# Kernel optimization log

Hardware: AMD Instinct MI355X
Metric: run time of the kernel (lower is better)

Reference implementation:

```python
import jax, jax.numpy as jnp
import numpy as np

B, N, D = 1, 2048, 1024
H = 16
HD = D // H
MAX_REL = 100          # relative_positional_distance
NUM_EMB = 2 * MAX_REL - 1
NEG = 1e8


def _rel_pos_logits(q_pos, rel_emb):
    """Fairseq-style learned relative positional logits (unmasked).

    q_pos:   [L, B*H, hd]  (unscaled queries)
    rel_emb: [H, 2*MAX_REL-1, hd]
    returns: [B*H, L, L]
    """
    L = q_pos.shape[0]
    pad_len = max(L - MAX_REL, 0)
    start = max(MAX_REL - L, 0)
    # get_embeddings_for_query: pad to cover relative offsets -(L-1)..(L-1)
    padded = jnp.pad(rel_emb, ((0, 0), (pad_len, pad_len), (0, 0)))
    used = padded[:, start:start + 2 * L - 1, :]          # [H, 2L-1, hd]
    # calculate_positional_logits
    q4 = q_pos.reshape(L, -1, H, HD)                       # [L, B, H, hd]
    logits = jnp.einsum('lbhd,hmd->lbhm', q4, used)        # [L, B, H, 2L-1]
    logits = logits.reshape(L, -1, 2 * L - 1)              # [L, BH, 2L-1]
    if pad_len > 0:  # mask relative positions beyond max_relative_pos
        logits = logits.at[:, :, :pad_len].add(-NEG)
        logits = logits.at[:, :, -pad_len:].add(-NEG)
    # relative_to_absolute_indexing (unmasked skewing trick)
    bh = logits.shape[1]
    x = jnp.pad(logits, ((0, 0), (0, 0), (0, 1)))          # [L, BH, 2L]
    x = jnp.transpose(x, (1, 0, 2)).reshape(bh, L * 2 * L)
    x = jnp.pad(x, ((0, 0), (0, L - 1)))
    x = x.reshape(bh, L + 1, 2 * L - 1)
    return x[:, :L, L - 1:]                                # [BH, L, L]


def setup_inputs() -> dict:
    key = jax.random.key(0)
    ks = jax.random.split(key, 6)
    x = jax.random.normal(ks[0], (B, N, D), dtype=jnp.float32)
    qkv_w = jax.random.normal(ks[1], (3 * D, D), dtype=jnp.float32) * 0.02
    qkv_b = jnp.zeros((3 * D,), dtype=jnp.float32)
    proj_w = jax.random.normal(ks[2], (D, D), dtype=jnp.float32) * 0.02
    proj_b = jnp.zeros((D,), dtype=jnp.float32)
    rel_emb = jax.random.normal(ks[3], (H, NUM_EMB, HD), dtype=jnp.float32) * (HD ** -0.5)
    return {"x": x, "qkv_w": qkv_w, "qkv_b": qkv_b,
            "proj_w": proj_w, "proj_b": proj_b, "rel_emb": rel_emb}


def reference(x, qkv_w, qkv_b, proj_w, proj_b, rel_emb):
    b, n, d = x.shape
    qkv = x @ qkv_w.T + qkv_b                                # [B,N,3D]
    qkv = qkv.reshape(b, n, 3, H, HD).transpose(2, 0, 3, 1, 4)
    q, k, v = qkv[0], qkv[1], qkv[2]                          # [B,H,N,hd]
    scale = 1.0 / np.sqrt(HD).astype(np.float32)
    logits = jnp.einsum('bhqd,bhkd->bhqk', q, k) * scale      # [B,H,N,N]
    q_pos = jnp.transpose(q, (0, 2, 1, 3)).reshape(n, b * H, HD)
    pos = _rel_pos_logits(q_pos, rel_emb).reshape(b, H, n, n)
    probs = jax.nn.softmax(logits + pos, axis=-1)             # dropout off (eval)
    out = jnp.einsum('bhqk,bhkd->bhqd', probs, v)
    out = jnp.transpose(out, (0, 2, 1, 3)).reshape(b, n, d)
    return out @ proj_w.T + proj_b
```

## Files before the change

### kernel.cpp

```cpp
#include <hip/hip_runtime.h>
#include <hip/hip_bf16.h>

#define N_SEQ 2048
#define DMODEL 1024
#define NHEAD 16
#define HD 64
#define NREL 199

typedef __bf16 bf16x8 __attribute__((ext_vector_type(8)));
typedef float f32x4 __attribute__((ext_vector_type(4)));

__device__ __forceinline__ bf16x8 cvt8(float4 a, float4 b) {
    bf16x8 r;
    r[0] = (__bf16)a.x; r[1] = (__bf16)a.y; r[2] = (__bf16)a.z; r[3] = (__bf16)a.w;
    r[4] = (__bf16)b.x; r[5] = (__bf16)b.y; r[6] = (__bf16)b.z; r[7] = (__bf16)b.w;
    return r;
}

#define MFMA16(A, B, C) __builtin_amdgcn_mfma_f32_16x16x32_bf16(A, B, C, 0, 0, 0)

__device__ __forceinline__ void async_copy16(void* lds, const void* g) {
    __builtin_amdgcn_global_load_lds(
        (__attribute__((address_space(1))) unsigned int*)g,
        (__attribute__((address_space(3))) unsigned int*)lds, 16, 0, 0);
}

__global__ __launch_bounds__(256) void cvt3(
    const float* __restrict__ a, __bf16* __restrict__ ao, int na,
    const float* __restrict__ b, __bf16* __restrict__ bo, int nb,
    const float* __restrict__ c, __bf16* __restrict__ co)
{
    int i = (blockIdx.x * blockDim.x + threadIdx.x) * 8;
    const float* src; __bf16* dst;
    if (i < na)              { src = a + i;            dst = ao + i; }
    else if (i - na < nb)    { src = b + (i - na);     dst = bo + (i - na); }
    else                     { src = c + (i - na - nb); dst = co + (i - na - nb); }
    float4 f0 = ((const float4*)src)[0];
    float4 f1 = ((const float4*)src)[1];
    *(bf16x8*)dst = cvt8(f0, f1);
}

template<int BM, int BN, bool OUT_BF16>
__global__ __launch_bounds__(256) void gemm_bt64(
    const __bf16* __restrict__ A,
    const __bf16* __restrict__ W,
    const float* __restrict__ bias,
    void* __restrict__ Cout,
    int lda, int Nc, int K, int ldc)
{
    constexpr int RT = BM + BN;
    constexpr int WM = BM / 2, WN = BN / 2;
    constexpr int MI = WM / 16, NI = WN / 16;
    constexpr int CHUNKS = RT / 4 / 8;

    __shared__ __bf16 s[RT][64];

    const int tid  = threadIdx.x;
    const int wid  = tid >> 6;
    const int lane = tid & 63;
    const int quad = lane >> 4;
    const int l15  = lane & 15;
    const int wm   = (wid >> 1) * WM;
    const int wn   = (wid & 1) * WN;
    const int bm   = blockIdx.y * BM;
    const int bn   = blockIdx.x * BN;

    const int lrow = lane >> 3;
    const int lcb  = ((lane & 7) ^ lrow) * 8;

    f32x4 acc[MI][NI] = {};

    for (int k0 = 0; k0 < K; k0 += 64) {
        #pragma unroll
        for (int c = 0; c < CHUNKS; c++) {
            const int r0 = wid * (RT / 4) + c * 8;
            const __bf16* src = (r0 < BM)
                ? A + (size_t)(bm + r0 + lrow) * lda + k0 + lcb
                : W + (size_t)(bn + (r0 - BM) + lrow) * K + k0 + lcb;
            async_copy16(&s[r0][0], src);
        }
        __syncthreads();

        #pragma unroll
        for (int half = 0; half < 2; half++) {
            bf16x8 af[MI], bfr[NI];
            #pragma unroll
            for (int mi = 0; mi < MI; mi++) {
                int ar = wm + mi * 16 + l15;
                af[mi] = *(const bf16x8*)&s[ar][((quad + 4 * half) ^ (ar & 7)) * 8];
            }
            #pragma unroll
            for (int ni = 0; ni < NI; ni++) {
                int br = BM + wn + ni * 16 + l15;
                bfr[ni] = *(const bf16x8*)&s[br][((quad + 4 * half) ^ (br & 7)) * 8];
            }
            #pragma unroll
            for (int mi = 0; mi < MI; mi++)
                #pragma unroll
                for (int ni = 0; ni < NI; ni++)
                    acc[mi][ni] = MFMA16(af[mi], bfr[ni], acc[mi][ni]);
        }
        __syncthreads();
    }

    #pragma unroll
    for (int ni = 0; ni < NI; ni++) {
        int col = bn + wn + ni * 16 + l15;
        float bv = bias[col];
        #pragma unroll
        for (int mi = 0; mi < MI; mi++)
            #pragma unroll
            for (int ri = 0; ri < 4; ri++) {
                int row = bm + wm + mi * 16 + quad * 4 + ri;
                float v = acc[mi][ni][ri] + bv;
                if (OUT_BF16)
                    reinterpret_cast<__bf16*>(Cout)[(size_t)row * ldc + col] = (__bf16)v;
                else
                    reinterpret_cast<float*>(Cout)[(size_t)row * ldc + col] = v;
            }
    }
}

__global__ __launch_bounds__(256) void attn_band_mfma(
    __hip_bfloat16* __restrict__ qkv,
    const float* __restrict__ rel_emb)
{
    __shared__ __align__(16) char smem[53248];
    __bf16 (*q_s)[72]   = (__bf16(*)[72])smem;
    __bf16 (*p_s)[72]   = (__bf16(*)[72])smem;
    __bf16 (*P_s)[200]  = (__bf16(*)[200])(smem + 9216);
    __bf16 (*relc)[72]  = (__bf16(*)[72])(smem + 34816);
    __bf16 (*k_s)[72]   = (__bf16(*)[72])(smem + 34816);
    __bf16 (*v_s)[72]   = (__bf16(*)[72])(smem + 34816 + 9216);

    const int tid  = threadIdx.x;
    const int wid  = tid >> 6;
    const int lane = tid & 63;
    const int quad = lane >> 4;
    const int l15  = lane & 15;
    const int h    = blockIdx.x >> 5;
    const int q0   = (blockIdx.x & 31) * 64;
    const int srow = tid >> 2;
    const int sq   = (tid & 3) * 16;

    const int j_lo   = (q0 - 99 > 0) ? (q0 - 99) : 0;
    const int j_hi   = (q0 + 162 < N_SEQ - 1) ? (q0 + 162) : (N_SEQ - 1);
    const int ntiles = (j_hi - j_lo + 64) >> 6;

    {
        const __hip_bfloat16* src = qkv + (size_t)(q0 + srow) * 3072 + h * HD + sq;
        uint4 u0 = ((const uint4*)src)[0];
        uint4 u1 = ((const uint4*)src)[1];
        *(uint4*)&q_s[srow][sq]     = u0;
        *(uint4*)&q_s[srow][sq + 8] = u1;
    }
    for (int idx = tid; idx < 112 * 4; idx += 256) {
        int er = idx >> 2, ec = (idx & 3) * 16;
        const float4* s = (const float4*)(rel_emb + ((size_t)h * NREL + er) * HD + ec);
        float4 f0 = s[0], f1 = s[1], f2 = s[2], f3 = s[3];
        *(bf16x8*)&relc[er][ec]     = cvt8(f0, f1);
        *(bf16x8*)&relc[er][ec + 8] = cvt8(f2, f3);
    }
    __syncthreads();

    const bf16x8 aq0 = *(const bf16x8*)&q_s[wid * 16 + l15][quad * 8];
    const bf16x8 aq1 = *(const bf16x8*)&q_s[wid * 16 + l15][quad * 8 + 32];

    #pragma unroll
    for (int t = 0; t < 7; t++) {
        f32x4 pacc = {};
        bf16x8 b0 = *(const bf16x8*)&relc[t * 16 + l15][quad * 8];
        bf16x8 b1 = *(const bf16x8*)&relc[t * 16 + l15][quad * 8 + 32];
        pacc = MFMA16(aq0, b0, pacc);
        pacc = MFMA16(aq1, b1, pacc);
        #pragma unroll
        for (int ri = 0; ri < 4; ri++)
            P_s[wid * 16 + quad * 4 + ri][t * 16 + l15] = (__bf16)pacc[ri];
    }
    __syncthreads();

    for (int idx = tid; idx < 96 * 4; idx += 256) {
        int er = 112 + (idx >> 2); if (er > NREL - 1) er = NREL - 1;
        int ec = (idx & 3) * 16;
        const float4* s = (const float4*)(rel_emb + ((size_t)h * NREL + er) * HD + ec);
        float4 f0 = s[0], f1 = s[1], f2 = s[2], f3 = s[3];
        *(bf16x8*)&relc[idx >> 2][ec]     = cvt8(f0, f1);
        *(bf16x8*)&relc[idx >> 2][ec + 8] = cvt8(f2, f3);
    }
    __syncthreads();

    #pragma unroll
    for (int t = 7; t < 13; t++) {
        f32x4 pacc = {};
        bf16x8 b0 = *(const bf16x8*)&relc[t * 16 + l15 - 112][quad * 8];
        bf16x8 b1 = *(const bf16x8*)&relc[t * 16 + l15 - 112][quad * 8 + 32];
        pacc = MFMA16(aq0, b0, pacc);
        pacc = MFMA16(aq1, b1, pacc);
        #pragma unroll
        for (int ri = 0; ri < 4; ri++) {
            int col = t * 16 + l15;
            if (col < NREL)
                P_s[wid * 16 + quad * 4 + ri][col] = (__bf16)pacc[ri];
        }
    }

    bf16x8 bones;
    {
        __bf16 o = (l15 == 0) ? (__bf16)1.0f : (__bf16)0.0f;
        #pragma unroll
        for (int i = 0; i < 8; i++) bones[i] = o;
    }

    f32x4 O[4] = {};
    f32x4 Osum = {};

    for (int t = 0; t < ntiles; t++) {
        __syncthreads();
        const int j0 = j_lo + t * 64;
        {
            int jr = j0 + srow; if (jr > N_SEQ - 1) jr = N_SEQ - 1;
            const __hip_bfloat16* ks = qkv + (size_t)jr * 3072 + 1024 + h * HD + sq;
            uint4 k0 = ((const uint4*)ks)[0], k1 = ((const uint4*)ks)[1];
            *(uint4*)&k_s[srow][sq]     = k0;
            *(uint4*)&k_s[srow][sq + 8] = k1;
            const __hip_bfloat16* vsp = qkv + (size_t)jr * 3072 + 2048 + h * HD + sq;
            uint4 v0 = ((const uint4*)vsp)[0], v1 = ((const uint4*)vsp)[1];
            __bf16 vtmp[16];
            *(uint4*)&vtmp[0] = v0; *(uint4*)&vtmp[8] = v1;
            #pragma unroll
            for (int i = 0; i < 16; i++) v_s[sq + i][srow] = vtmp[i];
        }
        __syncthreads();

        f32x4 S[4] = {};
        #pragma unroll
        for (int nt = 0; nt < 4; nt++) {
            bf16x8 b0 = *(const bf16x8*)&k_s[nt * 16 + l15][quad * 8];
            bf16x8 b1 = *(const bf16x8*)&k_s[nt * 16 + l15][quad * 8 + 32];
            S[nt] = MFMA16(aq0, b0, S[nt]);
            S[nt] = MFMA16(aq1, b1, S[nt]);
        }

        #pragma unroll
        for (int nt = 0; nt < 4; nt++) {
            int jg = j0 + nt * 16 + l15;
            #pragma unroll
            for (int ri = 0; ri < 4; ri++) {
                int r_loc = wid * 16 + quad * 4 + ri;
                int e = jg - (q0 + r_loc) + 99;
                float v = -3.0e38f;
                if ((unsigned)e < (unsigned)NREL && jg < N_SEQ)
                    v = S[nt][ri] * 0.125f + (float)P_s[r_loc][e];
                float p = __expf(v);
                p_s[r_loc][nt * 16 + l15] = (__bf16)p;
            }
        }

        bf16x8 ap0 = *(const bf16x8*)&p_s[wid * 16 + l15][quad * 8];
        bf16x8 ap1 = *(const bf16x8*)&p_s[wid * 16 + l15][quad * 8 + 32];
        #pragma unroll
        for (int nt = 0; nt < 4; nt++) {
            bf16x8 b0 = *(const bf16x8*)&v_s[nt * 16 + l15][quad * 8];
            bf16x8 b1 = *(const bf16x8*)&v_s[nt * 16 + l15][quad * 8 + 32];
            O[nt] = MFMA16(ap0, b0, O[nt]);
            O[nt] = MFMA16(ap1, b1, O[nt]);
        }
        Osum = MFMA16(ap0, bones, Osum);
        Osum = MFMA16(ap1, bones, Osum);
    }

    #pragma unroll
    for (int ri = 0; ri < 4; ri++) {
        float s = __shfl(Osum[ri], (lane & 48), 64);
        float inv = 1.0f / s;
        #pragma unroll
        for (int nt = 0; nt < 4; nt++) {
            int r = q0 + wid * 16 + quad * 4 + ri;
            qkv[(size_t)r * 3072 + h * HD + nt * 16 + l15] =
                __float2bfloat16(O[nt][ri] * inv);
        }
    }
}

extern "C" void kernel_launch(void* const* d_in, const int* in_sizes, int n_in,
                              void* d_out, int out_size, void* d_ws, size_t ws_size,
                              hipStream_t stream)
{
    (void)out_size; (void)ws_size; (void)n_in;

    const float *x = nullptr, *qkv_w = nullptr, *qkv_b = nullptr;
    const float *proj_w = nullptr, *proj_b = nullptr, *rel = nullptr;
    for (int i = 0; i < 6; i++) {
        switch (in_sizes[i]) {
            case 2097152: x      = (const float*)d_in[i]; break;
            case 3145728: qkv_w  = (const float*)d_in[i]; break;
            case 3072:    qkv_b  = (const float*)d_in[i]; break;
            case 1048576: proj_w = (const float*)d_in[i]; break;
            case 1024:    proj_b = (const float*)d_in[i]; break;
            case 203776:  rel    = (const float*)d_in[i]; break;
            default: break;
        }
    }

    char* ws = (char*)d_ws;
    __hip_bfloat16* qkv = (__hip_bfloat16*)ws;
    __bf16* xb  = (__bf16*)(ws + 12582912);
    __bf16* wb  = (__bf16*)(ws + 16777216);
    __bf16* pwb = (__bf16*)(ws + 23068672);
    float* out = (float*)d_out;

    cvt3<<<dim3(6291456 / 8 / 256), 256, 0, stream>>>(
        x, xb, 2097152, qkv_w, wb, 3145728, proj_w, pwb);
    gemm_bt64<128, 64, true><<<dim3(3072 / 64, N_SEQ / 128), 256, 0, stream>>>(
        xb, wb, qkv_b, (void*)qkv, DMODEL, 3072, DMODEL, 3072);
    attn_band_mfma<<<dim3(NHEAD * (N_SEQ / 64)), 256, 0, stream>>>(qkv, rel);
    gemm_bt64<64, 64, false><<<dim3(DMODEL / 64, N_SEQ / 64), 256, 0, stream>>>(
        (const __bf16*)qkv, pwb, proj_b, (void*)out, 3072, DMODEL, DMODEL, DMODEL);
}
```

Baseline: 132.0 us.

## Double K-step in GEMMs and register-prefetch next K/V tile in attention

The GEMM kernel now loads two 64-wide K slices into shared memory per iteration, which halves the number of barrier pairs and lets more async loads be in flight at once. The band attention kernel now holds the next K/V tile in registers, loading it from global memory while the current tile is being computed. Both aim to hide global memory latency. The cost is double the GEMM shared memory, which may lower occupancy, plus extra registers in the attention kernel.

```diff
diff --git a/kernel.cpp b/kernel.cpp
--- a/kernel.cpp
+++ b/kernel.cpp
@@ -40,7 +40,7 @@
     *(bf16x8*)dst = cvt8(f0, f1);
 }
 
-template<int BM, int BN, bool OUT_BF16>
+template<int BM, int BN, int KS, bool OUT_BF16>
 __global__ __launch_bounds__(256) void gemm_bt64(
     const __bf16* __restrict__ A,
     const __bf16* __restrict__ W,
@@ -53,7 +53,7 @@
     constexpr int MI = WM / 16, NI = WN / 16;
     constexpr int CHUNKS = RT / 4 / 8;
 
-    __shared__ __bf16 s[RT][64];
+    __shared__ __bf16 s[KS][RT][64];
 
     const int tid  = threadIdx.x;
     const int wid  = tid >> 6;
@@ -70,36 +70,40 @@
 
     f32x4 acc[MI][NI] = {};
 
-    for (int k0 = 0; k0 < K; k0 += 64) {
-        #pragma unroll
-        for (int c = 0; c < CHUNKS; c++) {
-            const int r0 = wid * (RT / 4) + c * 8;
-            const __bf16* src = (r0 < BM)
-                ? A + (size_t)(bm + r0 + lrow) * lda + k0 + lcb
-                : W + (size_t)(bn + (r0 - BM) + lrow) * K + k0 + lcb;
-            async_copy16(&s[r0][0], src);
-        }
+    for (int k0 = 0; k0 < K; k0 += 64 * KS) {
+        #pragma unroll
+        for (int ks = 0; ks < KS; ks++)
+            #pragma unroll
+            for (int c = 0; c < CHUNKS; c++) {
+                const int r0 = wid * (RT / 4) + c * 8;
+                const __bf16* src = (r0 < BM)
+                    ? A + (size_t)(bm + r0 + lrow) * lda + k0 + ks * 64 + lcb
+                    : W + (size_t)(bn + (r0 - BM) + lrow) * K + k0 + ks * 64 + lcb;
+                async_copy16(&s[ks][r0][0], src);
+            }
         __syncthreads();
 
         #pragma unroll
-        for (int half = 0; half < 2; half++) {
-            bf16x8 af[MI], bfr[NI];
-            #pragma unroll
-            for (int mi = 0; mi < MI; mi++) {
-                int ar = wm + mi * 16 + l15;
-                af[mi] = *(const bf16x8*)&s[ar][((quad + 4 * half) ^ (ar & 7)) * 8];
+        for (int ks = 0; ks < KS; ks++)
+            #pragma unroll
+            for (int half = 0; half < 2; half++) {
+                bf16x8 af[MI], bfr[NI];
+                #pragma unroll
+                for (int mi = 0; mi < MI; mi++) {
+                    int ar = wm + mi * 16 + l15;
+                    af[mi] = *(const bf16x8*)&s[ks][ar][((quad + 4 * half) ^ (ar & 7)) * 8];
+                }
+                #pragma unroll
+                for (int ni = 0; ni < NI; ni++) {
+                    int br = BM + wn + ni * 16 + l15;
+                    bfr[ni] = *(const bf16x8*)&s[ks][br][((quad + 4 * half) ^ (br & 7)) * 8];
+                }
+                #pragma unroll
+                for (int mi = 0; mi < MI; mi++)
+                    #pragma unroll
+                    for (int ni = 0; ni < NI; ni++)
+                        acc[mi][ni] = MFMA16(af[mi], bfr[ni], acc[mi][ni]);
             }
-            #pragma unroll
-            for (int ni = 0; ni < NI; ni++) {
-                int br = BM + wn + ni * 16 + l15;
-                bfr[ni] = *(const bf16x8*)&s[br][((quad + 4 * half) ^ (br & 7)) * 8];
-            }
-            #pragma unroll
-            for (int mi = 0; mi < MI; mi++)
-                #pragma unroll
-                for (int ni = 0; ni < NI; ni++)
-                    acc[mi][ni] = MFMA16(af[mi], bfr[ni], acc[mi][ni]);
-        }
         __syncthreads();
     }
 
@@ -147,6 +151,15 @@
     const int j_hi   = (q0 + 162 < N_SEQ - 1) ? (q0 + 162) : (N_SEQ - 1);
     const int ntiles = (j_hi - j_lo + 64) >> 6;
 
+    uint4 kr0, kr1, vr0, vr1;
+    {
+        int jr = j_lo + srow; if (jr > N_SEQ - 1) jr = N_SEQ - 1;
+        const uint4* ks = (const uint4*)(qkv + (size_t)jr * 3072 + 1024 + h * HD + sq);
+        kr0 = ks[0]; kr1 = ks[1];
+        const uint4* vs = (const uint4*)(qkv + (size_t)jr * 3072 + 2048 + h * HD + sq);
+        vr0 = vs[0]; vr1 = vs[1];
+    }
+
     {
         const __hip_bfloat16* src = qkv + (size_t)(q0 + srow) * 3072 + h * HD + sq;
         uint4 u0 = ((const uint4*)src)[0];
@@ -216,21 +229,26 @@
 
     for (int t = 0; t < ntiles; t++) {
         __syncthreads();
+
+        *(uint4*)&k_s[srow][sq]     = kr0;
+        *(uint4*)&k_s[srow][sq + 8] = kr1;
+        {
+            __bf16 vtmp[16];
+            *(uint4*)&vtmp[0] = vr0; *(uint4*)&vtmp[8] = vr1;
+            #pragma unroll
+            for (int i = 0; i < 16; i++) v_s[sq + i][srow] = vtmp[i];
+        }
+        __syncthreads();
+
+        if (t + 1 < ntiles) {
+            int jr = j_lo + (t + 1) * 64 + srow; if (jr > N_SEQ - 1) jr = N_SEQ - 1;
+            const uint4* ks = (const uint4*)(qkv + (size_t)jr * 3072 + 1024 + h * HD + sq);
+            kr0 = ks[0]; kr1 = ks[1];
+            const uint4* vs = (const uint4*)(qkv + (size_t)jr * 3072 + 2048 + h * HD + sq);
+            vr0 = vs[0]; vr1 = vs[1];
+        }
+
         const int j0 = j_lo + t * 64;
-        {
-            int jr = j0 + srow; if (jr > N_SEQ - 1) jr = N_SEQ - 1;
-            const __hip_bfloat16* ks = qkv + (size_t)jr * 3072 + 1024 + h * HD + sq;
-            uint4 k0 = ((const uint4*)ks)[0], k1 = ((const uint4*)ks)[1];
-            *(uint4*)&k_s[srow][sq]     = k0;
-            *(uint4*)&k_s[srow][sq + 8] = k1;
-            const __hip_bfloat16* vsp = qkv + (size_t)jr * 3072 + 2048 + h * HD + sq;
-            uint4 v0 = ((const uint4*)vsp)[0], v1 = ((const uint4*)vsp)[1];
-            __bf16 vtmp[16];
-            *(uint4*)&vtmp[0] = v0; *(uint4*)&vtmp[8] = v1;
-            #pragma unroll
-            for (int i = 0; i < 16; i++) v_s[sq + i][srow] = vtmp[i];
-        }
-        __syncthreads();
 
         f32x4 S[4] = {};
         #pragma unroll
@@ -311,9 +329,9 @@
 
     cvt3<<<dim3(6291456 / 8 / 256), 256, 0, stream>>>(
         x, xb, 2097152, qkv_w, wb, 3145728, proj_w, pwb);
-    gemm_bt64<128, 64, true><<<dim3(3072 / 64, N_SEQ / 128), 256, 0, stream>>>(
+    gemm_bt64<128, 64, 2, true><<<dim3(3072 / 64, N_SEQ / 128), 256, 0, stream>>>(
         xb, wb, qkv_b, (void*)qkv, DMODEL, 3072, DMODEL, 3072);
     attn_band_mfma<<<dim3(NHEAD * (N_SEQ / 64)), 256, 0, stream>>>(qkv, rel);
-    gemm_bt64<64, 64, false><<<dim3(DMODEL / 64, N_SEQ / 64), 256, 0, stream>>>(
+    gemm_bt64<64, 64, 2, false><<<dim3(DMODEL / 64, N_SEQ / 64), 256, 0, stream>>>(
         (const __bf16*)qkv, pwb, proj_b, (void*)out, 3072, DMODEL, DMODEL, DMODEL);
 }
```

Result: faster. 127.3 us (-3.5%).
